# Kernel optimization log

Hardware: AMD Instinct MI355X
Metric: run time of the kernel (lower is better)

## Reference

```python
import jax, jax.numpy as jnp
import numpy as np

S, D, P, R, E, M, K = 1024, 1024, 2816, 64, 8, 16, 1


def setup_inputs() -> dict:
    key = jax.random.key(0)
    ks = jax.random.split(key, 10)
    xav_a = (2.0 / (P + R)) ** 0.5   # xavier_uniform-like std for adapters
    xav_d = (2.0 / (D + P)) ** 0.5   # xavier for down projections
    bank_s = (1.0 / D) ** 0.5        # keep basis columns O(1)
    return {
        "hidden_states": jax.random.normal(ks[0], (S, D), jnp.float32),
        "expert_indices": jax.random.randint(ks[1], (S, K), 0, E),
        "expert_weights": jax.random.uniform(ks[2], (S, K), jnp.float32),
        "up_adapters": jax.random.normal(ks[3], (E, P, R), jnp.float32) * xav_a,
        "gate_adapters": jax.random.normal(ks[4], (E, P, R), jnp.float32) * xav_a,
        "up_mixture_logits": jax.random.normal(ks[5], (E, M), jnp.float32) * 0.01,
        "gate_mixture_logits": jax.random.normal(ks[6], (E, M), jnp.float32) * 0.01,
        "down_projections": jax.random.normal(ks[7], (E, D, P), jnp.float32) * xav_d,
        "up_bank": jax.random.normal(ks[8], (M, D, R), jnp.float32) * bank_s,
        "gate_bank": jax.random.normal(ks[9], (M, D, R), jnp.float32) * bank_s,
    }


def reference(hidden_states, expert_indices, expert_weights,
              up_adapters, gate_adapters, up_mixture_logits,
              gate_mixture_logits, down_projections, up_bank, gate_bank):
    n_experts = down_projections.shape[0]
    # SparseMixer: token-independent mixture weights over global bases (softmax)
    alpha_up = jax.nn.softmax(up_mixture_logits, axis=-1)      # [E, M]
    alpha_gate = jax.nn.softmax(gate_mixture_logits, axis=-1)  # [E, M]
    # Compose per-expert mixed bases: sum_j alpha_{e,j} B_j -> [E, D, R]
    up_mixed = jnp.einsum('em,mdr->edr', alpha_up, up_bank)
    gate_mixed = jnp.einsum('em,mdr->edr', alpha_gate, gate_bank)
    # Recomposed Up/Gate weights: A_e @ mixed_e^T -> [E, P, D]
    W_up = jnp.einsum('epr,edr->epd', up_adapters, up_mixed)
    W_gate = jnp.einsum('epr,edr->epd', gate_adapters, gate_mixed)
    # Combine routing weights per (token, expert): sum over topk slots
    onehot = (expert_indices[..., None] == jnp.arange(n_experts)).astype(hidden_states.dtype)  # [S,K,E]
    comb = jnp.einsum('ske,sk->se', onehot, expert_weights)  # [S, E]
    out = jnp.zeros_like(hidden_states)
    for e in range(n_experts):  # fixed small expert count
        up = hidden_states @ W_up[e].T        # [S, P]
        gate = hidden_states @ W_gate[e].T    # [S, P]
        inter = jax.nn.silu(gate) * up        # gated activation
        out = out + (inter @ down_projections[e].T) * comb[:, e:e + 1]
    return out
```

## Files before the change

kernel.cpp:

```cpp
#include <hip/hip_runtime.h>
#include <hip/hip_bf16.h>
#include <math.h>

#define S 1024
#define D 1024
#define P 2816
#define R 64
#define E 8
#define M 16
#define DSPLIT 8
#define KSPLIT 4
#define KQ (P / KSPLIT)
#define NIT (KQ / 64)

typedef __attribute__((ext_vector_type(8))) short short8;
typedef __attribute__((ext_vector_type(4))) float floatx4;

static __device__ inline unsigned short f2bf(float f) {
  __hip_bfloat16 h = __float2bfloat16(f);
  return *reinterpret_cast<unsigned short*>(&h);
}

__global__ __launch_bounds__(256) void k_pre(
    const float* __restrict__ up_logits, const float* __restrict__ gate_logits,
    const float* __restrict__ up_bank, const float* __restrict__ gate_bank,
    const int* __restrict__ idx,
    unsigned short* __restrict__ mxu, unsigned short* __restrict__ mxg,
    int* __restrict__ perm, int* __restrict__ offs, float* __restrict__ out) {
  int b = blockIdx.x, t = threadIdx.x;
  float4 z4 = make_float4(0.f, 0.f, 0.f, 0.f);
#pragma unroll
  for (int j = 0; j < 4; ++j)
    *(float4*)(out + (size_t)b * 4096 + j * 1024 + t * 4) = z4;

  if (b == 0) {
    __shared__ int hist[E];
    __shared__ int basearr[E];
    if (t < E) hist[t] = 0;
    __syncthreads();
    int e4[4];
#pragma unroll
    for (int j = 0; j < 4; ++j) {
      e4[j] = idx[t + j * 256];
      atomicAdd(&hist[e4[j]], 1);
    }
    __syncthreads();
    if (t == 0) {
      int run = 0;
      for (int i = 0; i < E; ++i) { basearr[i] = run; offs[i] = run; run += hist[i]; }
      offs[E] = S;
    }
    __syncthreads();
#pragma unroll
    for (int j = 0; j < 4; ++j) {
      int pos = atomicAdd(&basearr[e4[j]], 1);
      perm[pos] = t + j * 256;
    }
  }

  __shared__ float alpha[2][E][M];
  if (t < 16) {
    int mat = t >> 3, e = t & 7;
    const float* lg = (mat ? gate_logits : up_logits) + e * M;
    float v[M], mx = -1e30f, s = 0.f;
#pragma unroll
    for (int m = 0; m < M; ++m) { v[m] = lg[m]; mx = fmaxf(mx, v[m]); }
#pragma unroll
    for (int m = 0; m < M; ++m) { v[m] = expf(v[m] - mx); s += v[m]; }
#pragma unroll
    for (int m = 0; m < M; ++m) alpha[mat][e][m] = v[m] / s;
  }
  __syncthreads();
  int g = b * 256 + t;
  int d = g >> 6, r = g & 63;
  float au[E] = {0, 0, 0, 0, 0, 0, 0, 0}, ag[E] = {0, 0, 0, 0, 0, 0, 0, 0};
#pragma unroll
  for (int m = 0; m < M; ++m) {
    float vu = up_bank[((size_t)m * D + d) * R + r];
    float vg = gate_bank[((size_t)m * D + d) * R + r];
#pragma unroll
    for (int e = 0; e < E; ++e) {
      au[e] += alpha[0][e][m] * vu;
      ag[e] += alpha[1][e][m] * vg;
    }
  }
#pragma unroll
  for (int e = 0; e < E; ++e) {
    mxu[((size_t)e * D + d) * R + r] = f2bf(au[e]);
    mxg[((size_t)e * D + d) * R + r] = f2bf(ag[e]);
  }
}

__global__ __launch_bounds__(256) void k_t(
    const float* __restrict__ H, const unsigned short* __restrict__ mxu,
    const unsigned short* __restrict__ mxg, const int* __restrict__ perm,
    const int* __restrict__ offs, float* __restrict__ tpart) {
  int e = blockIdx.x;
  int start = offs[e] + blockIdx.y * 64;
  int end = offs[e + 1];
  if (start >= end) return;
  int z = blockIdx.z;
  __shared__ unsigned short As[64][72];
  __shared__ unsigned short Bs[128][72];
  int t = threadIdx.x;
  int lane = t & 63, w = t >> 6, quad = lane >> 4, l15 = lane & 15;
  int rows[2];
#pragma unroll
  for (int j = 0; j < 2; ++j) {
    int c = t + j * 256;
    int pos = start + (c >> 3);
    rows[j] = (pos < end) ? perm[pos] : -1;
  }
  floatx4 acc[8];
#pragma unroll
  for (int nt = 0; nt < 8; ++nt) acc[nt] = (floatx4){0.f, 0.f, 0.f, 0.f};

  for (int it = 0; it < 2; ++it) {
    int k0 = z * 128 + it * 64;
#pragma unroll
    for (int j = 0; j < 2; ++j) {
      int c = t + j * 256;
      int arow = c >> 3, acol = (c & 7) * 8;
      short8 v = (short8){0, 0, 0, 0, 0, 0, 0, 0};
      if (rows[j] >= 0) {
        const float* src = H + (size_t)rows[j] * D + k0 + acol;
        float4 f0 = *(const float4*)src;
        float4 f1 = *(const float4*)(src + 4);
        v[0] = f2bf(f0.x); v[1] = f2bf(f0.y); v[2] = f2bf(f0.z); v[3] = f2bf(f0.w);
        v[4] = f2bf(f1.x); v[5] = f2bf(f1.y); v[6] = f2bf(f1.z); v[7] = f2bf(f1.w);
      }
      *(short8*)&As[arow][acol] = v;
    }
    {
      int dd = t >> 2, r0 = (t & 3) * 16;
      const unsigned short* su = mxu + ((size_t)e * D + k0 + dd) * R + r0;
      const unsigned short* sg = mxg + ((size_t)e * D + k0 + dd) * R + r0;
      short8 u0 = *(const short8*)su, u1 = *(const short8*)(su + 8);
      short8 g0 = *(const short8*)sg, g1 = *(const short8*)(sg + 8);
#pragma unroll
      for (int j = 0; j < 8; ++j) {
        Bs[r0 + j][dd] = u0[j];
        Bs[r0 + 8 + j][dd] = u1[j];
        Bs[64 + r0 + j][dd] = g0[j];
        Bs[64 + r0 + 8 + j][dd] = g1[j];
      }
    }
    __syncthreads();
#pragma unroll
    for (int ks = 0; ks < 2; ++ks) {
      int kc = ks * 32 + quad * 8;
      short8 a = *(const short8*)&As[w * 16 + l15][kc];
#pragma unroll
      for (int nt = 0; nt < 8; ++nt) {
        short8 bb = *(const short8*)&Bs[nt * 16 + l15][kc];
        acc[nt] = __builtin_amdgcn_mfma_f32_16x16x32_bf16(a, bb, acc[nt], 0, 0, 0);
      }
    }
    __syncthreads();
  }
#pragma unroll
  for (int reg = 0; reg < 4; ++reg) {
    int pos = start + w * 16 + quad * 4 + reg;
    if (pos < end) {
#pragma unroll
      for (int nt = 0; nt < 8; ++nt)
        tpart[((size_t)z * S + pos) * 128 + nt * 16 + l15] = acc[nt][reg];
    }
  }
}

__global__ __launch_bounds__(256) void k_tred(
    const float* __restrict__ tpart, unsigned short* __restrict__ tbuf) {
  int i = blockIdx.x * 256 + threadIdx.x;
  float s = 0.f;
#pragma unroll
  for (int ds = 0; ds < DSPLIT; ++ds) s += tpart[(size_t)ds * S * 128 + i];
  tbuf[i] = f2bf(s);
}

__global__ __launch_bounds__(256) void k_inter(
    const unsigned short* __restrict__ tbuf, const float* __restrict__ Aup,
    const float* __restrict__ Agate, const int* __restrict__ offs,
    unsigned short* __restrict__ inter) {
  int e = blockIdx.x;
  int start = offs[e] + blockIdx.y * 64;
  int end = offs[e + 1];
  if (start >= end) return;
  int p0 = blockIdx.z * 128;
  __shared__ unsigned short Ts[64][136];
  __shared__ unsigned short Bu[128][72];
  __shared__ unsigned short Bg[128][72];
  int t = threadIdx.x;
  int lane = t & 63, w = t >> 6;
#pragma unroll
  for (int j = 0; j < 4; ++j) {
    int i = t + j * 256;
    int row = i >> 4, c8 = (i & 15) * 8;
    int pos = start + row;
    float4 v = (pos < end) ? *(const float4*)(tbuf + (size_t)pos * 128 + c8)
                           : make_float4(0.f, 0.f, 0.f, 0.f);
    *(float4*)&Ts[row][c8] = v;
  }
#pragma unroll
  for (int j = 0; j < 4; ++j) {
    int i = t + j * 256;
    int pr = i >> 3, c8 = (i & 7) * 8;
    const float* su = Aup + ((size_t)(e * P + p0 + pr) * R + c8);
    const float* sg = Agate + ((size_t)(e * P + p0 + pr) * R + c8);
    float4 u0 = *(const float4*)su, u1 = *(const float4*)(su + 4);
    float4 g0 = *(const float4*)sg, g1 = *(const float4*)(sg + 4);
    short8 uv, gv;
    uv[0] = f2bf(u0.x); uv[1] = f2bf(u0.y); uv[2] = f2bf(u0.z); uv[3] = f2bf(u0.w);
    uv[4] = f2bf(u1.x); uv[5] = f2bf(u1.y); uv[6] = f2bf(u1.z); uv[7] = f2bf(u1.w);
    gv[0] = f2bf(g0.x); gv[1] = f2bf(g0.y); gv[2] = f2bf(g0.z); gv[3] = f2bf(g0.w);
    gv[4] = f2bf(g1.x); gv[5] = f2bf(g1.y); gv[6] = f2bf(g1.z); gv[7] = f2bf(g1.w);
    *(short8*)&Bu[pr][c8] = uv;
    *(short8*)&Bg[pr][c8] = gv;
  }
  __syncthreads();
  int quad = lane >> 4, l15 = lane & 15;
  floatx4 au_acc[4][2], ag_acc[4][2];
#pragma unroll
  for (int tt = 0; tt < 4; ++tt)
#pragma unroll
    for (int pt = 0; pt < 2; ++pt) {
      au_acc[tt][pt] = (floatx4){0.f, 0.f, 0.f, 0.f};
      ag_acc[tt][pt] = (floatx4){0.f, 0.f, 0.f, 0.f};
    }
#pragma unroll
  for (int ks = 0; ks < 2; ++ks) {
    int kc = ks * 32 + quad * 8;
    short8 au[4], ag[4], bu[2], bg[2];
#pragma unroll
    for (int tt = 0; tt < 4; ++tt) {
      au[tt] = *(const short8*)&Ts[tt * 16 + l15][kc];
      ag[tt] = *(const short8*)&Ts[tt * 16 + l15][64 + kc];
    }
#pragma unroll
    for (int pt = 0; pt < 2; ++pt) {
      bu[pt] = *(const short8*)&Bu[w * 32 + pt * 16 + l15][kc];
      bg[pt] = *(const short8*)&Bg[w * 32 + pt * 16 + l15][kc];
    }
#pragma unroll
    for (int tt = 0; tt < 4; ++tt)
#pragma unroll
      for (int pt = 0; pt < 2; ++pt) {
        au_acc[tt][pt] = __builtin_amdgcn_mfma_f32_16x16x32_bf16(au[tt], bu[pt], au_acc[tt][pt], 0, 0, 0);
        ag_acc[tt][pt] = __builtin_amdgcn_mfma_f32_16x16x32_bf16(ag[tt], bg[pt], ag_acc[tt][pt], 0, 0, 0);
      }
  }
#pragma unroll
  for (int tt = 0; tt < 4; ++tt)
#pragma unroll
    for (int reg = 0; reg < 4; ++reg) {
      int row = tt * 16 + quad * 4 + reg;
      int pos = start + row;
      if (pos < end) {
#pragma unroll
        for (int pt = 0; pt < 2; ++pt) {
          float g = ag_acc[tt][pt][reg];
          float u = au_acc[tt][pt][reg];
          float val = u * (g / (1.f + __expf(-g)));
          inter[(size_t)pos * P + p0 + w * 32 + pt * 16 + l15] = f2bf(val);
        }
      }
    }
}

__global__ __launch_bounds__(256) void k_down(
    const unsigned short* __restrict__ inter, const float* __restrict__ Wd,
    const int* __restrict__ perm, const int* __restrict__ offs,
    const float* __restrict__ wts, float* __restrict__ out) {
  int e = blockIdx.x;
  int start = offs[e];
  int end = offs[e + 1];
  if (start >= end) return;
  int kz = blockIdx.y;
  int d0 = blockIdx.z * 64;
  __shared__ unsigned short As[256][72];
  __shared__ unsigned short Bs[64][72];
  int t = threadIdx.x;
  int lane = t & 63, w = t >> 6, quad = lane >> 4, l15 = lane & 15;

  const unsigned short* aptr[8];
  bool aok[8];
#pragma unroll
  for (int j = 0; j < 8; ++j) {
    int arow = (t >> 3) + 32 * j;
    int pos = start + arow;
    aok[j] = (pos < end);
    aptr[j] = inter + (size_t)(aok[j] ? pos : start) * P + kz * KQ + (t & 7) * 8;
  }
  const float* bsrc = Wd + ((size_t)(e * D + d0 + (t >> 2)) * P + kz * KQ + (t & 3) * 16);

  float4 pa[8];
  float4 pb[4];
#pragma unroll
  for (int j = 0; j < 8; ++j)
    pa[j] = aok[j] ? *(const float4*)(aptr[j]) : make_float4(0.f, 0.f, 0.f, 0.f);
#pragma unroll
  for (int q = 0; q < 4; ++q) pb[q] = *(const float4*)(bsrc + q * 4);

  floatx4 acc[4][4];
#pragma unroll
  for (int tt = 0; tt < 4; ++tt)
#pragma unroll
    for (int dt = 0; dt < 4; ++dt) acc[tt][dt] = (floatx4){0.f, 0.f, 0.f, 0.f};

  for (int it = 0; it < NIT; ++it) {
#pragma unroll
    for (int j = 0; j < 8; ++j)
      *(float4*)&As[(t >> 3) + 32 * j][(t & 7) * 8] = pa[j];
    {
      short8 bv0, bv1;
      bv0[0] = f2bf(pb[0].x); bv0[1] = f2bf(pb[0].y); bv0[2] = f2bf(pb[0].z); bv0[3] = f2bf(pb[0].w);
      bv0[4] = f2bf(pb[1].x); bv0[5] = f2bf(pb[1].y); bv0[6] = f2bf(pb[1].z); bv0[7] = f2bf(pb[1].w);
      bv1[0] = f2bf(pb[2].x); bv1[1] = f2bf(pb[2].y); bv1[2] = f2bf(pb[2].z); bv1[3] = f2bf(pb[2].w);
      bv1[4] = f2bf(pb[3].x); bv1[5] = f2bf(pb[3].y); bv1[6] = f2bf(pb[3].z); bv1[7] = f2bf(pb[3].w);
      *(short8*)&Bs[t >> 2][(t & 3) * 16] = bv0;
      *(short8*)&Bs[t >> 2][(t & 3) * 16 + 8] = bv1;
    }
    __syncthreads();
    if (it + 1 < NIT) {
      int k0 = (it + 1) * 64;
#pragma unroll
      for (int j = 0; j < 8; ++j)
        pa[j] = aok[j] ? *(const float4*)(aptr[j] + k0) : make_float4(0.f, 0.f, 0.f, 0.f);
#pragma unroll
      for (int q = 0; q < 4; ++q) pb[q] = *(const float4*)(bsrc + k0 + q * 4);
    }
#pragma unroll
    for (int ks = 0; ks < 2; ++ks) {
      int kc = ks * 32 + quad * 8;
      short8 a[4], b[4];
#pragma unroll
      for (int tt = 0; tt < 4; ++tt) a[tt] = *(const short8*)&As[w * 64 + tt * 16 + l15][kc];
#pragma unroll
      for (int dt = 0; dt < 4; ++dt) b[dt] = *(const short8*)&Bs[dt * 16 + l15][kc];
#pragma unroll
      for (int tt = 0; tt < 4; ++tt)
#pragma unroll
        for (int dt = 0; dt < 4; ++dt)
          acc[tt][dt] = __builtin_amdgcn_mfma_f32_16x16x32_bf16(a[tt], b[dt], acc[tt][dt], 0, 0, 0);
    }
    __syncthreads();
  }
#pragma unroll
  for (int tt = 0; tt < 4; ++tt)
#pragma unroll
    for (int reg = 0; reg < 4; ++reg) {
      int pos = start + w * 64 + tt * 16 + quad * 4 + reg;
      if (pos < end) {
        int tok = perm[pos];
        float wt = wts[tok];
#pragma unroll
        for (int dt = 0; dt < 4; ++dt)
          atomicAdd(&out[(size_t)tok * D + d0 + dt * 16 + l15], acc[tt][dt][reg] * wt);
      }
    }
}

extern "C" void kernel_launch(void* const* d_in, const int* in_sizes, int n_in,
                              void* d_out, int out_size, void* d_ws, size_t ws_size,
                              hipStream_t stream) {
  const float* H = (const float*)d_in[0];
  const int* idx = (const int*)d_in[1];
  const float* wts = (const float*)d_in[2];
  const float* Aup = (const float*)d_in[3];
  const float* Agate = (const float*)d_in[4];
  const float* upl = (const float*)d_in[5];
  const float* gatel = (const float*)d_in[6];
  const float* Wd = (const float*)d_in[7];
  const float* upb = (const float*)d_in[8];
  const float* gateb = (const float*)d_in[9];
  float* out = (float*)d_out;

  char* ws = (char*)d_ws;
  unsigned short* mxu = (unsigned short*)ws;
  unsigned short* mxg = mxu + (size_t)E * D * R;
  float* tpart = (float*)(mxg + (size_t)E * D * R);
  unsigned short* tbuf = (unsigned short*)(tpart + (size_t)DSPLIT * S * 128);
  unsigned short* inter = tbuf + (size_t)S * 128;
  int* perm = (int*)(inter + (size_t)S * P);
  int* offs = perm + S;

  k_pre<<<256, 256, 0, stream>>>(upl, gatel, upb, gateb, idx, mxu, mxg, perm, offs, out);
  k_t<<<dim3(E, 4, DSPLIT), 256, 0, stream>>>(H, mxu, mxg, perm, offs, tpart);
  k_tred<<<512, 256, 0, stream>>>(tpart, tbuf);
  k_inter<<<dim3(E, 4, P / 128), 256, 0, stream>>>(tbuf, Aup, Agate, offs, inter);
  k_down<<<dim3(E, KSPLIT, D / 64), 256, 0, stream>>>(inter, Wd, perm, offs, wts, out);
}
```

Measured before the change: 213.1 us.

## Pre-convert operands to bf16, drop reduction kernel, retile inter/down grids

Measured after the change: 259.5 us. 21.7% more time.

```diff
diff --git a/kernel.cpp b/kernel.cpp
--- a/kernel.cpp
+++ b/kernel.cpp
@@ -8,10 +8,11 @@
 #define R 64
 #define E 8
 #define M 16
-#define DSPLIT 8
 #define KSPLIT 4
 #define KQ (P / KSPLIT)
 #define NIT (KQ / 64)
+#define ZT 16
+#define ACH ((E * P * R) / 8)
 
 typedef __attribute__((ext_vector_type(8))) short short8;
 typedef __attribute__((ext_vector_type(4))) float floatx4;
@@ -20,18 +21,29 @@
   __hip_bfloat16 h = __float2bfloat16(f);
   return *reinterpret_cast<unsigned short*>(&h);
 }
+static __device__ inline short8 pack8(float4 a, float4 b) {
+  short8 v;
+  v[0] = f2bf(a.x); v[1] = f2bf(a.y); v[2] = f2bf(a.z); v[3] = f2bf(a.w);
+  v[4] = f2bf(b.x); v[5] = f2bf(b.y); v[6] = f2bf(b.z); v[7] = f2bf(b.w);
+  return v;
+}
 
 __global__ __launch_bounds__(256) void k_pre(
     const float* __restrict__ up_logits, const float* __restrict__ gate_logits,
     const float* __restrict__ up_bank, const float* __restrict__ gate_bank,
-    const int* __restrict__ idx,
-    unsigned short* __restrict__ mxu, unsigned short* __restrict__ mxg,
-    int* __restrict__ perm, int* __restrict__ offs, float* __restrict__ out) {
+    const float* __restrict__ H, const float* __restrict__ Aup,
+    const float* __restrict__ Agate, const int* __restrict__ idx,
+    unsigned short* __restrict__ Hbf, unsigned short* __restrict__ mxT,
+    unsigned short* __restrict__ Aubf, unsigned short* __restrict__ Agbf,
+    int* __restrict__ perm, int* __restrict__ offs,
+    float* __restrict__ tbuf, float* __restrict__ out) {
   int b = blockIdx.x, t = threadIdx.x;
+  int g = b * 256 + t;
   float4 z4 = make_float4(0.f, 0.f, 0.f, 0.f);
 #pragma unroll
   for (int j = 0; j < 4; ++j)
     *(float4*)(out + (size_t)b * 4096 + j * 1024 + t * 4) = z4;
+  *(float2*)(tbuf + (size_t)g * 2) = make_float2(0.f, 0.f);
 
   if (b == 0) {
     __shared__ int hist[E];
@@ -55,6 +67,26 @@
     for (int j = 0; j < 4; ++j) {
       int pos = atomicAdd(&basearr[e4[j]], 1);
       perm[pos] = t + j * 256;
+    }
+  }
+
+  {
+    const float* hs = H + (size_t)g * 16;
+    float4 h0 = *(const float4*)hs, h1 = *(const float4*)(hs + 4);
+    float4 h2 = *(const float4*)(hs + 8), h3 = *(const float4*)(hs + 12);
+    *(short8*)(Hbf + (size_t)g * 16) = pack8(h0, h1);
+    *(short8*)(Hbf + (size_t)g * 16 + 8) = pack8(h2, h3);
+  }
+#pragma unroll
+  for (int j = 0; j < 3; ++j) {
+    int c = g + j * 65536;
+    if (c < ACH) {
+      const float* su = Aup + (size_t)c * 8;
+      const float* sg = Agate + (size_t)c * 8;
+      float4 u0 = *(const float4*)su, u1 = *(const float4*)(su + 4);
+      float4 g0 = *(const float4*)sg, g1 = *(const float4*)(sg + 4);
+      *(short8*)(Aubf + (size_t)c * 8) = pack8(u0, u1);
+      *(short8*)(Agbf + (size_t)c * 8) = pack8(g0, g1);
     }
   }
 
@@ -71,7 +103,6 @@
     for (int m = 0; m < M; ++m) alpha[mat][e][m] = v[m] / s;
   }
   __syncthreads();
-  int g = b * 256 + t;
   int d = g >> 6, r = g & 63;
   float au[E] = {0, 0, 0, 0, 0, 0, 0, 0}, ag[E] = {0, 0, 0, 0, 0, 0, 0, 0};
 #pragma unroll
@@ -86,183 +117,97 @@
   }
 #pragma unroll
   for (int e = 0; e < E; ++e) {
-    mxu[((size_t)e * D + d) * R + r] = f2bf(au[e]);
-    mxg[((size_t)e * D + d) * R + r] = f2bf(ag[e]);
+    mxT[((size_t)e * 128 + r) * D + d] = f2bf(au[e]);
+    mxT[((size_t)e * 128 + 64 + r) * D + d] = f2bf(ag[e]);
   }
 }
 
 __global__ __launch_bounds__(256) void k_t(
-    const float* __restrict__ H, const unsigned short* __restrict__ mxu,
-    const unsigned short* __restrict__ mxg, const int* __restrict__ perm,
-    const int* __restrict__ offs, float* __restrict__ tpart) {
+    const unsigned short* __restrict__ Hbf, const unsigned short* __restrict__ mxT,
+    const int* __restrict__ perm, const int* __restrict__ offs,
+    float* __restrict__ tbuf) {
   int e = blockIdx.x;
-  int start = offs[e] + blockIdx.y * 64;
+  int end = offs[e + 1];
+  int t = threadIdx.x, lane = t & 63, w = t >> 6;
+  int quad = lane >> 4, l15 = lane & 15;
+  int row0 = offs[e] + blockIdx.y * 64 + w * 16;
+  if (row0 >= end) return;
+  int k0 = blockIdx.z * (D / ZT);
+  int pos = row0 + l15;
+  int tok = (pos < end) ? perm[pos] : -1;
+  const unsigned short* hrow = Hbf + (size_t)(tok < 0 ? 0 : tok) * D + k0;
+  floatx4 acc[8];
+#pragma unroll
+  for (int nt = 0; nt < 8; ++nt) acc[nt] = (floatx4){0.f, 0.f, 0.f, 0.f};
+#pragma unroll
+  for (int ks = 0; ks < 2; ++ks) {
+    int kc = ks * 32 + quad * 8;
+    short8 a = (short8){0, 0, 0, 0, 0, 0, 0, 0};
+    if (tok >= 0) a = *(const short8*)(hrow + kc);
+#pragma unroll
+    for (int nt = 0; nt < 8; ++nt) {
+      short8 bb = *(const short8*)(mxT + ((size_t)e * 128 + nt * 16 + l15) * D + k0 + kc);
+      acc[nt] = __builtin_amdgcn_mfma_f32_16x16x32_bf16(a, bb, acc[nt], 0, 0, 0);
+    }
+  }
+#pragma unroll
+  for (int reg = 0; reg < 4; ++reg) {
+    int p = row0 + quad * 4 + reg;
+    if (p < end) {
+#pragma unroll
+      for (int nt = 0; nt < 8; ++nt)
+        atomicAdd(&tbuf[(size_t)p * 128 + nt * 16 + l15], acc[nt][reg]);
+    }
+  }
+}
+
+__global__ __launch_bounds__(256) void k_inter(
+    const float* __restrict__ tbuf, const unsigned short* __restrict__ Aubf,
+    const unsigned short* __restrict__ Agbf, const int* __restrict__ offs,
+    unsigned short* __restrict__ inter) {
+  int e = blockIdx.x;
+  int start = offs[e] + blockIdx.y * 16;
   int end = offs[e + 1];
   if (start >= end) return;
-  int z = blockIdx.z;
-  __shared__ unsigned short As[64][72];
-  __shared__ unsigned short Bs[128][72];
-  int t = threadIdx.x;
-  int lane = t & 63, w = t >> 6, quad = lane >> 4, l15 = lane & 15;
-  int rows[2];
-#pragma unroll
-  for (int j = 0; j < 2; ++j) {
-    int c = t + j * 256;
-    int pos = start + (c >> 3);
-    rows[j] = (pos < end) ? perm[pos] : -1;
-  }
-  floatx4 acc[8];
-#pragma unroll
-  for (int nt = 0; nt < 8; ++nt) acc[nt] = (floatx4){0.f, 0.f, 0.f, 0.f};
-
-  for (int it = 0; it < 2; ++it) {
-    int k0 = z * 128 + it * 64;
-#pragma unroll
-    for (int j = 0; j < 2; ++j) {
-      int c = t + j * 256;
-      int arow = c >> 3, acol = (c & 7) * 8;
-      short8 v = (short8){0, 0, 0, 0, 0, 0, 0, 0};
-      if (rows[j] >= 0) {
-        const float* src = H + (size_t)rows[j] * D + k0 + acol;
-        float4 f0 = *(const float4*)src;
-        float4 f1 = *(const float4*)(src + 4);
-        v[0] = f2bf(f0.x); v[1] = f2bf(f0.y); v[2] = f2bf(f0.z); v[3] = f2bf(f0.w);
-        v[4] = f2bf(f1.x); v[5] = f2bf(f1.y); v[6] = f2bf(f1.z); v[7] = f2bf(f1.w);
-      }
-      *(short8*)&As[arow][acol] = v;
-    }
-    {
-      int dd = t >> 2, r0 = (t & 3) * 16;
-      const unsigned short* su = mxu + ((size_t)e * D + k0 + dd) * R + r0;
-      const unsigned short* sg = mxg + ((size_t)e * D + k0 + dd) * R + r0;
-      short8 u0 = *(const short8*)su, u1 = *(const short8*)(su + 8);
-      short8 g0 = *(const short8*)sg, g1 = *(const short8*)(sg + 8);
-#pragma unroll
-      for (int j = 0; j < 8; ++j) {
-        Bs[r0 + j][dd] = u0[j];
-        Bs[r0 + 8 + j][dd] = u1[j];
-        Bs[64 + r0 + j][dd] = g0[j];
-        Bs[64 + r0 + 8 + j][dd] = g1[j];
-      }
-    }
-    __syncthreads();
-#pragma unroll
-    for (int ks = 0; ks < 2; ++ks) {
-      int kc = ks * 32 + quad * 8;
-      short8 a = *(const short8*)&As[w * 16 + l15][kc];
-#pragma unroll
-      for (int nt = 0; nt < 8; ++nt) {
-        short8 bb = *(const short8*)&Bs[nt * 16 + l15][kc];
-        acc[nt] = __builtin_amdgcn_mfma_f32_16x16x32_bf16(a, bb, acc[nt], 0, 0, 0);
-      }
-    }
-    __syncthreads();
-  }
-#pragma unroll
-  for (int reg = 0; reg < 4; ++reg) {
-    int pos = start + w * 16 + quad * 4 + reg;
-    if (pos < end) {
-#pragma unroll
-      for (int nt = 0; nt < 8; ++nt)
-        tpart[((size_t)z * S + pos) * 128 + nt * 16 + l15] = acc[nt][reg];
-    }
-  }
-}
-
-__global__ __launch_bounds__(256) void k_tred(
-    const float* __restrict__ tpart, unsigned short* __restrict__ tbuf) {
-  int i = blockIdx.x * 256 + threadIdx.x;
-  float s = 0.f;
-#pragma unroll
-  for (int ds = 0; ds < DSPLIT; ++ds) s += tpart[(size_t)ds * S * 128 + i];
-  tbuf[i] = f2bf(s);
-}
-
-__global__ __launch_bounds__(256) void k_inter(
-    const unsigned short* __restrict__ tbuf, const float* __restrict__ Aup,
-    const float* __restrict__ Agate, const int* __restrict__ offs,
-    unsigned short* __restrict__ inter) {
-  int e = blockIdx.x;
-  int start = offs[e] + blockIdx.y * 64;
-  int end = offs[e + 1];
-  if (start >= end) return;
-  int p0 = blockIdx.z * 128;
-  __shared__ unsigned short Ts[64][136];
-  __shared__ unsigned short Bu[128][72];
-  __shared__ unsigned short Bg[128][72];
-  int t = threadIdx.x;
-  int lane = t & 63, w = t >> 6;
-#pragma unroll
-  for (int j = 0; j < 4; ++j) {
-    int i = t + j * 256;
-    int row = i >> 4, c8 = (i & 15) * 8;
-    int pos = start + row;
-    float4 v = (pos < end) ? *(const float4*)(tbuf + (size_t)pos * 128 + c8)
-                           : make_float4(0.f, 0.f, 0.f, 0.f);
-    *(float4*)&Ts[row][c8] = v;
-  }
-#pragma unroll
-  for (int j = 0; j < 4; ++j) {
-    int i = t + j * 256;
-    int pr = i >> 3, c8 = (i & 7) * 8;
-    const float* su = Aup + ((size_t)(e * P + p0 + pr) * R + c8);
-    const float* sg = Agate + ((size_t)(e * P + p0 + pr) * R + c8);
-    float4 u0 = *(const float4*)su, u1 = *(const float4*)(su + 4);
-    float4 g0 = *(const float4*)sg, g1 = *(const float4*)(sg + 4);
-    short8 uv, gv;
-    uv[0] = f2bf(u0.x); uv[1] = f2bf(u0.y); uv[2] = f2bf(u0.z); uv[3] = f2bf(u0.w);
-    uv[4] = f2bf(u1.x); uv[5] = f2bf(u1.y); uv[6] = f2bf(u1.z); uv[7] = f2bf(u1.w);
-    gv[0] = f2bf(g0.x); gv[1] = f2bf(g0.y); gv[2] = f2bf(g0.z); gv[3] = f2bf(g0.w);
-    gv[4] = f2bf(g1.x); gv[5] = f2bf(g1.y); gv[6] = f2bf(g1.z); gv[7] = f2bf(g1.w);
-    *(short8*)&Bu[pr][c8] = uv;
-    *(short8*)&Bg[pr][c8] = gv;
-  }
-  __syncthreads();
+  int t = threadIdx.x, lane = t & 63, w = t >> 6;
   int quad = lane >> 4, l15 = lane & 15;
-  floatx4 au_acc[4][2], ag_acc[4][2];
-#pragma unroll
-  for (int tt = 0; tt < 4; ++tt)
-#pragma unroll
-    for (int pt = 0; pt < 2; ++pt) {
-      au_acc[tt][pt] = (floatx4){0.f, 0.f, 0.f, 0.f};
-      ag_acc[tt][pt] = (floatx4){0.f, 0.f, 0.f, 0.f};
-    }
+  int p0 = blockIdx.z * 256 + w * 64;
+  int pos = start + l15;
+  bool okA = pos < end;
+  floatx4 accu[4], accg[4];
+#pragma unroll
+  for (int nt = 0; nt < 4; ++nt) {
+    accu[nt] = (floatx4){0.f, 0.f, 0.f, 0.f};
+    accg[nt] = (floatx4){0.f, 0.f, 0.f, 0.f};
+  }
 #pragma unroll
   for (int ks = 0; ks < 2; ++ks) {
     int kc = ks * 32 + quad * 8;
-    short8 au[4], ag[4], bu[2], bg[2];
-#pragma unroll
-    for (int tt = 0; tt < 4; ++tt) {
-      au[tt] = *(const short8*)&Ts[tt * 16 + l15][kc];
-      ag[tt] = *(const short8*)&Ts[tt * 16 + l15][64 + kc];
-    }
-#pragma unroll
-    for (int pt = 0; pt < 2; ++pt) {
-      bu[pt] = *(const short8*)&Bu[w * 32 + pt * 16 + l15][kc];
-      bg[pt] = *(const short8*)&Bg[w * 32 + pt * 16 + l15][kc];
-    }
-#pragma unroll
-    for (int tt = 0; tt < 4; ++tt)
-#pragma unroll
-      for (int pt = 0; pt < 2; ++pt) {
-        au_acc[tt][pt] = __builtin_amdgcn_mfma_f32_16x16x32_bf16(au[tt], bu[pt], au_acc[tt][pt], 0, 0, 0);
-        ag_acc[tt][pt] = __builtin_amdgcn_mfma_f32_16x16x32_bf16(ag[tt], bg[pt], ag_acc[tt][pt], 0, 0, 0);
-      }
-  }
-#pragma unroll
-  for (int tt = 0; tt < 4; ++tt)
+    short8 au = (short8){0, 0, 0, 0, 0, 0, 0, 0};
+    short8 ag = (short8){0, 0, 0, 0, 0, 0, 0, 0};
+    if (okA) {
+      const float* tp = tbuf + (size_t)pos * 128 + kc;
+      au = pack8(*(const float4*)tp, *(const float4*)(tp + 4));
+      ag = pack8(*(const float4*)(tp + 64), *(const float4*)(tp + 68));
+    }
+#pragma unroll
+    for (int nt = 0; nt < 4; ++nt) {
+      size_t prow = (size_t)e * P + p0 + nt * 16 + l15;
+      short8 bu = *(const short8*)(Aubf + prow * R + kc);
+      short8 bg = *(const short8*)(Agbf + prow * R + kc);
+      accu[nt] = __builtin_amdgcn_mfma_f32_16x16x32_bf16(au, bu, accu[nt], 0, 0, 0);
+      accg[nt] = __builtin_amdgcn_mfma_f32_16x16x32_bf16(ag, bg, accg[nt], 0, 0, 0);
+    }
+  }
+#pragma unroll
+  for (int nt = 0; nt < 4; ++nt)
 #pragma unroll
     for (int reg = 0; reg < 4; ++reg) {
-      int row = tt * 16 + quad * 4 + reg;
-      int pos = start + row;
-      if (pos < end) {
-#pragma unroll
-        for (int pt = 0; pt < 2; ++pt) {
-          float g = ag_acc[tt][pt][reg];
-          float u = au_acc[tt][pt][reg];
-          float val = u * (g / (1.f + __expf(-g)));
-          inter[(size_t)pos * P + p0 + w * 32 + pt * 16 + l15] = f2bf(val);
-        }
+      int prow = start + quad * 4 + reg;
+      if (prow < end) {
+        float gv = accg[nt][reg], uv = accu[nt][reg];
+        float val = uv * (gv / (1.f + __expf(-gv)));
+        inter[(size_t)prow * P + p0 + nt * 16 + l15] = f2bf(val);
       }
     }
 }
@@ -272,92 +217,68 @@
     const int* __restrict__ perm, const int* __restrict__ offs,
     const float* __restrict__ wts, float* __restrict__ out) {
   int e = blockIdx.x;
-  int start = offs[e];
+  int start = offs[e] + blockIdx.y * 64;
   int end = offs[e + 1];
   if (start >= end) return;
-  int kz = blockIdx.y;
-  int d0 = blockIdx.z * 64;
-  __shared__ unsigned short As[256][72];
+  int kz = blockIdx.z >> 4;
+  int d0 = (blockIdx.z & 15) * 64;
+  __shared__ unsigned short As[64][72];
   __shared__ unsigned short Bs[64][72];
   int t = threadIdx.x;
   int lane = t & 63, w = t >> 6, quad = lane >> 4, l15 = lane & 15;
 
-  const unsigned short* aptr[8];
-  bool aok[8];
-#pragma unroll
-  for (int j = 0; j < 8; ++j) {
-    int arow = (t >> 3) + 32 * j;
-    int pos = start + arow;
-    aok[j] = (pos < end);
-    aptr[j] = inter + (size_t)(aok[j] ? pos : start) * P + kz * KQ + (t & 7) * 8;
-  }
-  const float* bsrc = Wd + ((size_t)(e * D + d0 + (t >> 2)) * P + kz * KQ + (t & 3) * 16);
-
-  float4 pa[8];
+  int arow = t >> 2;
+  int apos = start + arow;
+  bool aok = apos < end;
+  const unsigned short* aptr =
+      inter + (size_t)(aok ? apos : start) * P + kz * KQ + (t & 3) * 16;
+  const float* bptr = Wd + ((size_t)(e * D + d0 + (t >> 2)) * P + kz * KQ + (t & 3) * 16);
+
+  short8 pa0 = (short8){0, 0, 0, 0, 0, 0, 0, 0}, pa1 = pa0;
   float4 pb[4];
-#pragma unroll
-  for (int j = 0; j < 8; ++j)
-    pa[j] = aok[j] ? *(const float4*)(aptr[j]) : make_float4(0.f, 0.f, 0.f, 0.f);
-#pragma unroll
-  for (int q = 0; q < 4; ++q) pb[q] = *(const float4*)(bsrc + q * 4);
-
-  floatx4 acc[4][4];
-#pragma unroll
-  for (int tt = 0; tt < 4; ++tt)
-#pragma unroll
-    for (int dt = 0; dt < 4; ++dt) acc[tt][dt] = (floatx4){0.f, 0.f, 0.f, 0.f};
+  if (aok) { pa0 = *(const short8*)aptr; pa1 = *(const short8*)(aptr + 8); }
+#pragma unroll
+  for (int q = 0; q < 4; ++q) pb[q] = *(const float4*)(bptr + q * 4);
+
+  floatx4 acc[4];
+#pragma unroll
+  for (int dt = 0; dt < 4; ++dt) acc[dt] = (floatx4){0.f, 0.f, 0.f, 0.f};
 
   for (int it = 0; it < NIT; ++it) {
-#pragma unroll
-    for (int j = 0; j < 8; ++j)
-      *(float4*)&As[(t >> 3) + 32 * j][(t & 7) * 8] = pa[j];
-    {
-      short8 bv0, bv1;
-      bv0[0] = f2bf(pb[0].x); bv0[1] = f2bf(pb[0].y); bv0[2] = f2bf(pb[0].z); bv0[3] = f2bf(pb[0].w);
-      bv0[4] = f2bf(pb[1].x); bv0[5] = f2bf(pb[1].y); bv0[6] = f2bf(pb[1].z); bv0[7] = f2bf(pb[1].w);
-      bv1[0] = f2bf(pb[2].x); bv1[1] = f2bf(pb[2].y); bv1[2] = f2bf(pb[2].z); bv1[3] = f2bf(pb[2].w);
-      bv1[4] = f2bf(pb[3].x); bv1[5] = f2bf(pb[3].y); bv1[6] = f2bf(pb[3].z); bv1[7] = f2bf(pb[3].w);
-      *(short8*)&Bs[t >> 2][(t & 3) * 16] = bv0;
-      *(short8*)&Bs[t >> 2][(t & 3) * 16 + 8] = bv1;
-    }
+    *(short8*)&As[arow][(t & 3) * 16] = pa0;
+    *(short8*)&As[arow][(t & 3) * 16 + 8] = pa1;
+    *(short8*)&Bs[t >> 2][(t & 3) * 16] = pack8(pb[0], pb[1]);
+    *(short8*)&Bs[t >> 2][(t & 3) * 16 + 8] = pack8(pb[2], pb[3]);
     __syncthreads();
     if (it + 1 < NIT) {
       int k0 = (it + 1) * 64;
-#pragma unroll
-      for (int j = 0; j < 8; ++j)
-        pa[j] = aok[j] ? *(const float4*)(aptr[j] + k0) : make_float4(0.f, 0.f, 0.f, 0.f);
-#pragma unroll
-      for (int q = 0; q < 4; ++q) pb[q] = *(const float4*)(bsrc + k0 + q * 4);
+      if (aok) { pa0 = *(const short8*)(aptr + k0); pa1 = *(const short8*)(aptr + k0 + 8); }
+#pragma unroll
+      for (int q = 0; q < 4; ++q) pb[q] = *(const float4*)(bptr + k0 + q * 4);
     }
 #pragma unroll
     for (int ks = 0; ks < 2; ++ks) {
       int kc = ks * 32 + quad * 8;
-      short8 a[4], b[4];
-#pragma unroll
-      for (int tt = 0; tt < 4; ++tt) a[tt] = *(const short8*)&As[w * 64 + tt * 16 + l15][kc];
-#pragma unroll
-      for (int dt = 0; dt < 4; ++dt) b[dt] = *(const short8*)&Bs[dt * 16 + l15][kc];
-#pragma unroll
-      for (int tt = 0; tt < 4; ++tt)
-#pragma unroll
-        for (int dt = 0; dt < 4; ++dt)
-          acc[tt][dt] = __builtin_amdgcn_mfma_f32_16x16x32_bf16(a[tt], b[dt], acc[tt][dt], 0, 0, 0);
-    }
-    __syncthreads();
-  }
-#pragma unroll
-  for (int tt = 0; tt < 4; ++tt)
-#pragma unroll
-    for (int reg = 0; reg < 4; ++reg) {
-      int pos = start + w * 64 + tt * 16 + quad * 4 + reg;
-      if (pos < end) {
-        int tok = perm[pos];
-        float wt = wts[tok];
-#pragma unroll
-        for (int dt = 0; dt < 4; ++dt)
-          atomicAdd(&out[(size_t)tok * D + d0 + dt * 16 + l15], acc[tt][dt][reg] * wt);
+      short8 a = *(const short8*)&As[w * 16 + l15][kc];
+#pragma unroll
+      for (int dt = 0; dt < 4; ++dt) {
+        short8 b = *(const short8*)&Bs[dt * 16 + l15][kc];
+        acc[dt] = __builtin_amdgcn_mfma_f32_16x16x32_bf16(a, b, acc[dt], 0, 0, 0);
       }
     }
+    __syncthreads();
+  }
+#pragma unroll
+  for (int reg = 0; reg < 4; ++reg) {
+    int pos = start + w * 16 + quad * 4 + reg;
+    if (pos < end) {
+      int tok = perm[pos];
+      float wt = wts[tok];
+#pragma unroll
+      for (int dt = 0; dt < 4; ++dt)
+        atomicAdd(&out[(size_t)tok * D + d0 + dt * 16 + l15], acc[dt][reg] * wt);
+    }
+  }
 }
 
 extern "C" void kernel_launch(void* const* d_in, const int* in_sizes, int n_in,
@@ -376,17 +297,18 @@
   float* out = (float*)d_out;
 
   char* ws = (char*)d_ws;
-  unsigned short* mxu = (unsigned short*)ws;
-  unsigned short* mxg = mxu + (size_t)E * D * R;
-  float* tpart = (float*)(mxg + (size_t)E * D * R);
-  unsigned short* tbuf = (unsigned short*)(tpart + (size_t)DSPLIT * S * 128);
-  unsigned short* inter = tbuf + (size_t)S * 128;
-  int* perm = (int*)(inter + (size_t)S * P);
+  unsigned short* Hbf = (unsigned short*)ws;
+  unsigned short* mxT = Hbf + (size_t)S * D;
+  unsigned short* Aubf = mxT + (size_t)E * 128 * D;
+  unsigned short* Agbf = Aubf + (size_t)E * P * R;
+  unsigned short* inter = Agbf + (size_t)E * P * R;
+  float* tbuf = (float*)(inter + (size_t)S * P);
+  int* perm = (int*)(tbuf + (size_t)S * 128);
   int* offs = perm + S;
 
-  k_pre<<<256, 256, 0, stream>>>(upl, gatel, upb, gateb, idx, mxu, mxg, perm, offs, out);
-  k_t<<<dim3(E, 4, DSPLIT), 256, 0, stream>>>(H, mxu, mxg, perm, offs, tpart);
-  k_tred<<<512, 256, 0, stream>>>(tpart, tbuf);
-  k_inter<<<dim3(E, 4, P / 128), 256, 0, stream>>>(tbuf, Aup, Agate, offs, inter);
-  k_down<<<dim3(E, KSPLIT, D / 64), 256, 0, stream>>>(inter, Wd, perm, offs, wts, out);
-}
+  k_pre<<<256, 256, 0, stream>>>(upl, gatel, upb, gateb, H, Aup, Agate, idx,
+                                 Hbf, mxT, Aubf, Agbf, perm, offs, tbuf, out);
+  k_t<<<dim3(E, 4, ZT), 256, 0, stream>>>(Hbf, mxT, perm, offs, tbuf);
+  k_inter<<<dim3(E, 16, P / 256), 256, 0, stream>>>(tbuf, Aubf, Agbf, offs, inter);
+  k_down<<<dim3(E, 4, KSPLIT * 16), 256, 0, stream>>>(inter, Wd, perm, offs, wts, out);
+}
```
